# Performance work log

Measured on AMD Instinct MI355X. Metric: run time of the kernel, lower is better.

## Reference

```python
import jax, jax.numpy as jnp
import numpy as np

N, C, T, V = 16, 64, 512, 25
R, O, S = 8, 64, 3  # rel_channels, out_channels, num_subset


def setup_inputs() -> dict:
    key = jax.random.key(0)
    ks = jax.random.split(key, 12)
    sc = 0.05
    return {
        "x": jax.random.normal(ks[0], (N, C, T, V), jnp.float32),
        "A": jax.random.normal(ks[1], (S, V, V), jnp.float32) * 0.1,
        "alpha": jax.random.normal(ks[2], (1,), jnp.float32) * 0.1,
        "w1": jax.random.normal(ks[3], (S, R, C), jnp.float32) * sc,
        "b1": jax.random.normal(ks[4], (S, R), jnp.float32) * sc,
        "w2": jax.random.normal(ks[5], (S, R, C), jnp.float32) * sc,
        "b2": jax.random.normal(ks[6], (S, R), jnp.float32) * sc,
        "w3": jax.random.normal(ks[7], (S, O, C), jnp.float32) * sc,
        "b3": jax.random.normal(ks[8], (S, O), jnp.float32) * sc,
        "w4": jax.random.normal(ks[9], (S, O, R), jnp.float32) * sc,
        "b4": jax.random.normal(ks[10], (S, O), jnp.float32) * sc,
        "sparse": 0,
    }


def _mask(w, thr):
    # SparseConv2d: magnitude-threshold the 1x1 conv weights at runtime.
    return jnp.where(jnp.abs(w) > thr, w, jnp.zeros_like(w))


def reference(x, A, alpha, w1, b1, w2, b2, w3, b3, w4, b4, sparse):
    thr = jnp.float32(sparse)

    def conv1x1(w, b, inp):  # w [o,c], b [o], inp [n,c,t,v] -> [n,o,t,v]
        return jnp.einsum('oc,nctv->notv', _mask(w, thr), inp) + b[None, :, None, None]

    y = None
    for i in range(A.shape[0]):
        x1 = conv1x1(w1[i], b1[i], x).mean(-2)          # [n,r,v]
        x2 = conv1x1(w2[i], b2[i], x).mean(-2)          # [n,r,v]
        x3 = conv1x1(w3[i], b3[i], x)                   # [n,o,t,v]
        att = jnp.tanh(x1[..., :, None] - x2[..., None, :])  # [n,r,v,v]
        a = jnp.einsum('or,nruv->nouv', _mask(w4[i], thr), att) + b4[i][None, :, None, None]
        a = a * alpha + A[i][None, None]                # [n,o,v,v]
        z = jnp.einsum('ncuv,nctu->nctv', a, x3)        # node aggregation
        y = z if y is None else y + z
    # in_channels == out_channels -> residual is identity
    return jax.nn.relu(y + x)
```

## Files before the change

### kernel.cpp

```cpp
#include <hip/hip_runtime.h>
#include <cmath>

typedef __bf16 bf16x4v __attribute__((ext_vector_type(4)));
typedef __bf16 bf16x8 __attribute__((ext_vector_type(8)));
typedef float f32x4 __attribute__((ext_vector_type(4)));

namespace {
constexpr int kN = 16, kC = 64, kT = 512, kV = 25, kS = 3, kO = 64;
constexpr int kTV = kT * kV;
constexpr size_t WS_AFRAG = 102400;
constexpr size_t WS_W3F = WS_AFRAG + (size_t)48 * 131072;
constexpr size_t WS_XBF = WS_W3F + 3 * 8192;
}

__device__ __forceinline__ int swzB16(int c, int t, int ubyte) {
  return (c << 10) + (((t << 6) + ubyte) ^ ((((c ^ t) & 7)) << 4));
}

__global__ __launch_bounds__(256) void k1_cvt(const float* __restrict__ x,
                                              __bf16* __restrict__ xbf,
                                              float* __restrict__ xm) {
  const int bid = blockIdx.x;
  __shared__ float part[250][4];
  const int tid = threadIdx.x;
  const float4* xg4 = (const float4*)(x + (size_t)bid * kTV);
  bf16x4v* xb4 = (bf16x4v*)(xbf + (size_t)bid * kTV);
  if (tid < 250) {
    float a0 = 0.f, a1 = 0.f, a2 = 0.f, a3 = 0.f;
    for (int j = tid; j < 3200; j += 250) {
      float4 v = xg4[j];
      a0 += v.x; a1 += v.y; a2 += v.z; a3 += v.w;
      bf16x4v o;
      o[0] = (__bf16)v.x; o[1] = (__bf16)v.y;
      o[2] = (__bf16)v.z; o[3] = (__bf16)v.w;
      xb4[j] = o;
    }
    part[tid][0] = a0; part[tid][1] = a1; part[tid][2] = a2; part[tid][3] = a3;
  }
  __syncthreads();
  if (tid < 25) {
    float s = 0.f;
#pragma unroll
    for (int r = 0; r < 4; ++r) {
      int q = ((tid - r + 25) % 25) * 19 % 25;
#pragma unroll
      for (int p = 0; p < 10; ++p) s += part[q + 25 * p][r];
    }
    xm[bid * 25 + tid] = s * (1.f / 512.f);
  }
}

__global__ __launch_bounds__(256) void k2_attn(
    const float* __restrict__ xm, const float* __restrict__ Ag,
    const float* __restrict__ alpha, const float* __restrict__ w1,
    const float* __restrict__ b1, const float* __restrict__ w2,
    const float* __restrict__ b2, const float* __restrict__ w3,
    const float* __restrict__ w4, const float* __restrict__ b4,
    const int* __restrict__ sparse, unsigned char* __restrict__ ws) {
  const float thr = (float)sparse[0];
  const int b = blockIdx.x;
  const int s = b >> 6, n = (b >> 2) & 15, q = b & 3;
  __shared__ float xm_l[1600];
  __shared__ float x1_l[200], x2_l[200];
  __shared__ float att_l[8 * 625];
  __shared__ float attsum_l[200];
  __shared__ float ag_l[625];
  __shared__ float acs_l[25];
  __shared__ float w4_l[512];
  const int tid = threadIdx.x;
  for (int i = tid; i < 1600; i += 256) xm_l[i] = xm[n * 1600 + i];
  for (int i = tid; i < 512; i += 256) {
    float w = w4[s * 512 + i];
    w4_l[i] = (fabsf(w) > thr) ? w : 0.f;
  }
  for (int i = tid; i < 625; i += 256) ag_l[i] = Ag[s * 625 + i];
  __syncthreads();
  for (int i = tid; i < 400; i += 256) {
    int which = i / 200, idx = i % 200, r = idx / 25, u = idx % 25;
    const float* wrow = (which == 0 ? w1 : w2) + (s * 8 + r) * 64;
    float acc = 0.f;
    for (int cc = 0; cc < 64; ++cc) {
      float w = wrow[cc];
      w = (fabsf(w) > thr) ? w : 0.f;
      acc += w * xm_l[cc * 25 + u];
    }
    acc += (which == 0 ? b1 : b2)[s * 8 + r];
    if (which == 0) x1_l[idx] = acc;
    else x2_l[idx] = acc;
  }
  __syncthreads();
  for (int i = tid; i < 8 * 625; i += 256) {
    int r = i / 625, uv = i % 625, u = uv / 25, v = uv % 25;
    att_l[i] = tanhf(x1_l[r * 25 + u] - x2_l[r * 25 + v]);
  }
  __syncthreads();
  if (tid < 200) {
    int r = tid / 25, v = tid % 25;
    float sum = 0.f;
    for (int u = 0; u < 25; ++u) sum += att_l[r * 625 + u * 25 + v];
    attsum_l[tid] = sum;
  } else if (tid < 225) {
    int v = tid - 200;
    float sum = 0.f;
    for (int u = 0; u < 25; ++u) sum += ag_l[u * 25 + v];
    acs_l[v] = sum;
  }
  __syncthreads();
  const float al = alpha[0];
  unsigned char* afrag = ws + WS_AFRAG + (size_t)(s * 16 + n) * 131072;
  for (int slot = q * 2048 + tid; slot < (q + 1) * 2048; slot += 256) {
    int c = slot >> 7, vt = (slot >> 6) & 1, l = slot & 63;
    int v = vt * 16 + (l & 15), g = l >> 4;
    bf16x8 out;
    if (v < 25) {
      float b4v = b4[s * 64 + c];
#pragma unroll
      for (int j = 0; j < 8; ++j) {
        int u = g * 8 + j;
        float val = 0.f;
        if (u < 25) {
          float acc = 0.f;
#pragma unroll
          for (int r = 0; r < 8; ++r) acc += w4_l[c * 8 + r] * att_l[r * 625 + u * 25 + v];
          val = al * (acc + b4v) + ag_l[u * 25 + v];
        } else if (u == 25) {
          float acc = 0.f;
#pragma unroll
          for (int r = 0; r < 8; ++r) acc += w4_l[c * 8 + r] * attsum_l[r * 25 + v];
          val = al * acc + 25.f * al * b4v + acs_l[v];
        }
        out[j] = (__bf16)val;
      }
    } else {
#pragma unroll
      for (int j = 0; j < 8; ++j) out[j] = (__bf16)0.f;
    }
    *(bf16x8*)(afrag + (size_t)slot * 16) = out;
  }
  if (n == 0 && tid < 128) {
    unsigned char* w3f = ws + WS_W3F + (size_t)s * 8192;
    int slot = q * 128 + tid;
    int ot = slot >> 7, ks = (slot >> 6) & 1, l = slot & 63;
    int o = ot * 16 + (l & 15), g = l >> 4;
    bf16x8 out;
#pragma unroll
    for (int j = 0; j < 8; ++j) {
      int cp = ks * 32 + g * 8 + j;
      float w = w3[(s * 64 + o) * 64 + cp];
      out[j] = (__bf16)((fabsf(w) > thr) ? w : 0.f);
    }
    *(bf16x8*)(w3f + slot * 16) = out;
  }
}

__global__ __launch_bounds__(512) void k3_main(const __bf16* __restrict__ xbf,
                                               const float* __restrict__ b3,
                                               const unsigned char* __restrict__ ws,
                                               float* __restrict__ y) {
  const int n = blockIdx.x;
  const int tb = blockIdx.y;
  extern __shared__ __align__(16) unsigned char smem[];
  const int tid = threadIdx.x;
  const int w = tid >> 6, l = tid & 63, g = l >> 4, l15 = l & 15;

  {
    const f32x4* src = (const f32x4*)(ws + WS_W3F);
    f32x4* dst = (f32x4*)(smem + 65536);
    for (int i = tid; i < 1536; i += 512) dst[i] = src[i];
  }
  for (int idx = tid; idx < 3072; idx += 512) {
    int pair = idx / 3, k = idx % 3;
    int c = pair >> 4, t = pair & 15;
    *(unsigned int*)(smem + swzB16(c, t, 52 + 4 * k)) = 0u;
  }

  bf16x8 xa[4][2];
#pragma unroll
  for (int cti = 0; cti < 4; ++cti)
#pragma unroll
    for (int kf = 0; kf < 2; ++kf)
#pragma unroll
      for (int j = 0; j < 8; ++j) xa[cti][kf][j] = (__bf16)0.f;
  {
    const __bf16* xbp = xbf + (size_t)n * kC * kTV;
#pragma unroll
    for (int cti = 0; cti < 4; ++cti) {
      int tt = tb * 16 + 2 * w + (cti >> 1);
      int u = (cti & 1) * 16 + l15;
      if (u < 25) {
#pragma unroll
        for (int kf = 0; kf < 2; ++kf)
#pragma unroll
          for (int j = 0; j < 8; ++j) {
            int cp = kf * 32 + g * 8 + j;
            xa[cti][kf][j] = xbp[(size_t)cp * kTV + tt * 25 + u];
          }
      }
    }
  }
  __syncthreads();

  const unsigned char* afrag = ws + WS_AFRAG;

  f32x4 zacc[8][2];
#pragma unroll
  for (int cc = 0; cc < 8; ++cc)
#pragma unroll
    for (int vt = 0; vt < 2; ++vt) {
      f32x4 zz = {0.f, 0.f, 0.f, 0.f};
      zacc[cc][vt] = zz;
    }

  for (int s = 0; s < kS; ++s) {
    bf16x8 B2[8][2];
    const unsigned char* af = afrag + (size_t)(s * 16 + n) * 131072;
#pragma unroll
    for (int cc = 0; cc < 8; ++cc) {
      int c = w * 8 + cc;
#pragma unroll
      for (int vt = 0; vt < 2; ++vt)
        B2[cc][vt] = *(const bf16x8*)(af + ((c * 2 + vt) * 64 + l) * 16);
    }
    if (s) __syncthreads();

    const unsigned char* w3l = smem + 65536 + s * 8192;
#pragma unroll
    for (int ot = 0; ot < 4; ++ot) {
      bf16x8 wk0 = *(const bf16x8*)(w3l + ((ot * 2 + 0) * 64 + l) * 16);
      bf16x8 wk1 = *(const bf16x8*)(w3l + ((ot * 2 + 1) * 64 + l) * 16);
      int c = ot * 16 + l15;
#pragma unroll
      for (int cti = 0; cti < 4; ++cti) {
        f32x4 d = {0.f, 0.f, 0.f, 0.f};
        d = __builtin_amdgcn_mfma_f32_16x16x32_bf16(xa[cti][0], wk0, d, 0, 0, 0);
        d = __builtin_amdgcn_mfma_f32_16x16x32_bf16(xa[cti][1], wk1, d, 0, 0, 0);
        int tt = 2 * w + (cti >> 1);
        if (!(cti & 1)) {
          bf16x4v pk;
          pk[0] = (__bf16)d[0]; pk[1] = (__bf16)d[1];
          pk[2] = (__bf16)d[2]; pk[3] = (__bf16)d[3];
          *(bf16x4v*)(smem + swzB16(c, tt, g * 8)) = pk;
        } else if (g < 2) {
          bf16x4v pk;
          pk[0] = (__bf16)d[0]; pk[1] = (__bf16)d[1];
          pk[2] = (__bf16)d[2]; pk[3] = (__bf16)d[3];
          *(bf16x4v*)(smem + swzB16(c, tt, 32 + g * 8)) = pk;
        } else if (g == 2) {
          *(__bf16*)(smem + swzB16(c, tt, 48)) = (__bf16)d[0];
        }
      }
    }
    for (int i = tid; i < 1024; i += 512) {
      int c = i >> 4, t = i & 15;
      *(__bf16*)(smem + swzB16(c, t, 50)) = (__bf16)b3[s * 64 + c];
    }
    __syncthreads();
#pragma unroll
    for (int cc = 0; cc < 8; ++cc) {
      int c = w * 8 + cc;
      bf16x8 a2 = *(const bf16x8*)(smem + swzB16(c, l15, g * 16));
      zacc[cc][0] = __builtin_amdgcn_mfma_f32_16x16x32_bf16(a2, B2[cc][0], zacc[cc][0], 0, 0, 0);
      zacc[cc][1] = __builtin_amdgcn_mfma_f32_16x16x32_bf16(a2, B2[cc][1], zacc[cc][1], 0, 0, 0);
    }
  }
  __syncthreads();
  float* zs = (float*)smem;
  const __bf16* xbp = xbf + (size_t)n * kC * kTV;
  float4* yg4 = (float4*)(y + (size_t)n * kC * kTV);
#pragma unroll
  for (int h = 0; h < 2; ++h) {
    if ((w >> 2) == h) {
      int c0l = (w & 3) * 8;
#pragma unroll
      for (int cc = 0; cc < 8; ++cc)
#pragma unroll
        for (int vt = 0; vt < 2; ++vt) {
          int v = vt * 16 + l15;
          if (v < 25) {
#pragma unroll
            for (int jj = 0; jj < 4; ++jj)
              zs[(c0l + cc) * 400 + (g * 4 + jj) * 25 + v] = zacc[cc][vt][jj];
          }
        }
    }
    __syncthreads();
    for (int i4 = tid; i4 < 3200; i4 += 512) {
      int cl = i4 / 100, r4 = i4 % 100, c = h * 32 + cl;
      bf16x4v xv = *(const bf16x4v*)(xbp + (size_t)c * kTV + tb * 400 + r4 * 4);
      f32x4 zv = *(const f32x4*)(zs + cl * 400 + r4 * 4);
      float4 o;
      o.x = fmaxf(zv[0] + (float)xv[0], 0.f);
      o.y = fmaxf(zv[1] + (float)xv[1], 0.f);
      o.z = fmaxf(zv[2] + (float)xv[2], 0.f);
      o.w = fmaxf(zv[3] + (float)xv[3], 0.f);
      yg4[c * 3200 + tb * 100 + r4] = o;
    }
    __syncthreads();
  }
}

extern "C" void kernel_launch(void* const* d_in, const int* in_sizes, int n_in,
                              void* d_out, int out_size, void* d_ws, size_t ws_size,
                              hipStream_t stream) {
  const float* x = (const float*)d_in[0];
  const float* Ag = (const float*)d_in[1];
  const float* alpha = (const float*)d_in[2];
  const float* w1 = (const float*)d_in[3];
  const float* b1 = (const float*)d_in[4];
  const float* w2 = (const float*)d_in[5];
  const float* b2 = (const float*)d_in[6];
  const float* w3 = (const float*)d_in[7];
  const float* b3 = (const float*)d_in[8];
  const float* w4 = (const float*)d_in[9];
  const float* b4 = (const float*)d_in[10];
  const int* sparse = (const int*)d_in[11];

  unsigned char* ws = (unsigned char*)d_ws;
  float* xm = (float*)ws;
  __bf16* xbf = (__bf16*)(ws + WS_XBF);
  float* y = (float*)d_out;

  hipFuncSetAttribute((const void*)k3_main,
                      hipFuncAttributeMaxDynamicSharedMemorySize, 90112);

  k1_cvt<<<kN * kC, 256, 0, stream>>>(x, xbf, xm);
  k2_attn<<<kS * kN * 4, 256, 0, stream>>>(xm, Ag, alpha, w1, b1, w2, b2, w3, w4,
                                           b4, sparse, ws);
  dim3 g3(kN, kT / 16);
  k3_main<<<g3, 512, 90112, stream>>>(xbf, b3, ws, y);
}
```

Before: 74.68 us.

## Transpose x to channel-contiguous bf16 layout for vectorized MFMA operand loads

New measurement: 86.41 us. 15.7% more time.

```diff
diff --git a/kernel.cpp b/kernel.cpp
--- a/kernel.cpp
+++ b/kernel.cpp
@@ -10,53 +10,58 @@
 constexpr int kTV = kT * kV;
 constexpr size_t WS_AFRAG = 102400;
 constexpr size_t WS_W3F = WS_AFRAG + (size_t)48 * 131072;
-constexpr size_t WS_XBF = WS_W3F + 3 * 8192;
+constexpr size_t WS_XTR = WS_W3F + 3 * 8192;
+constexpr size_t WS_PSUM = WS_XTR + (size_t)16 * 819200 * 2 + 4096;
 }
 
 __device__ __forceinline__ int swzB16(int c, int t, int ubyte) {
   return (c << 10) + (((t << 6) + ubyte) ^ ((((c ^ t) & 7)) << 4));
 }
 
-__global__ __launch_bounds__(256) void k1_cvt(const float* __restrict__ x,
-                                              __bf16* __restrict__ xbf,
-                                              float* __restrict__ xm) {
-  const int bid = blockIdx.x;
-  __shared__ float part[250][4];
+__global__ __launch_bounds__(512) void k1_tr(const float* __restrict__ x,
+                                             unsigned char* __restrict__ ws) {
+  const int n = blockIdx.x, tc = blockIdx.y;
+  extern __shared__ __align__(16) unsigned char sm1[];
+  __bf16* tile = (__bf16*)sm1;
   const int tid = threadIdx.x;
-  const float4* xg4 = (const float4*)(x + (size_t)bid * kTV);
-  bf16x4v* xb4 = (bf16x4v*)(xbf + (size_t)bid * kTV);
-  if (tid < 250) {
-    float a0 = 0.f, a1 = 0.f, a2 = 0.f, a3 = 0.f;
-    for (int j = tid; j < 3200; j += 250) {
-      float4 v = xg4[j];
-      a0 += v.x; a1 += v.y; a2 += v.z; a3 += v.w;
-      bf16x4v o;
-      o[0] = (__bf16)v.x; o[1] = (__bf16)v.y;
-      o[2] = (__bf16)v.z; o[3] = (__bf16)v.w;
-      xb4[j] = o;
-    }
-    part[tid][0] = a0; part[tid][1] = a1; part[tid][2] = a2; part[tid][3] = a3;
-  }
-  __syncthreads();
-  if (tid < 25) {
+  const float4* xg4 = (const float4*)(x + (size_t)n * kC * kTV);
+  for (int i4 = tid; i4 < 12800; i4 += 512) {
+    int c = i4 / 200, r = i4 % 200;
+    float4 v = xg4[c * 3200 + tc * 200 + r];
+    bf16x4v o;
+    o[0] = (__bf16)v.x; o[1] = (__bf16)v.y;
+    o[2] = (__bf16)v.z; o[3] = (__bf16)v.w;
+    *(bf16x4v*)(tile + c * 800 + r * 4) = o;
+  }
+  __syncthreads();
+  __bf16* xtr = (__bf16*)(ws + WS_XTR) + (size_t)n * 819200 + (size_t)tc * 51200;
+  for (int col = tid; col < 800; col += 512) {
+    __bf16* dst = xtr + (size_t)col * 64;
+#pragma unroll
+    for (int cb = 0; cb < 8; ++cb) {
+      bf16x8 pk;
+#pragma unroll
+      for (int j = 0; j < 8; ++j) pk[j] = tile[(cb * 8 + j) * 800 + col];
+      *(bf16x8*)(dst + cb * 8) = pk;
+    }
+  }
+  float* psum = (float*)(ws + WS_PSUM);
+  for (int i = tid; i < 1600; i += 512) {
+    int c = i / 25, v = i % 25;
     float s = 0.f;
 #pragma unroll
-    for (int r = 0; r < 4; ++r) {
-      int q = ((tid - r + 25) % 25) * 19 % 25;
-#pragma unroll
-      for (int p = 0; p < 10; ++p) s += part[q + 25 * p][r];
-    }
-    xm[bid * 25 + tid] = s * (1.f / 512.f);
+    for (int t = 0; t < 32; ++t) s += (float)tile[c * 800 + t * 25 + v];
+    psum[((size_t)n * 1600 + i) * 16 + tc] = s;
   }
 }
 
 __global__ __launch_bounds__(256) void k2_attn(
-    const float* __restrict__ xm, const float* __restrict__ Ag,
-    const float* __restrict__ alpha, const float* __restrict__ w1,
-    const float* __restrict__ b1, const float* __restrict__ w2,
-    const float* __restrict__ b2, const float* __restrict__ w3,
-    const float* __restrict__ w4, const float* __restrict__ b4,
-    const int* __restrict__ sparse, unsigned char* __restrict__ ws) {
+    const float* __restrict__ Ag, const float* __restrict__ alpha,
+    const float* __restrict__ w1, const float* __restrict__ b1,
+    const float* __restrict__ w2, const float* __restrict__ b2,
+    const float* __restrict__ w3, const float* __restrict__ w4,
+    const float* __restrict__ b4, const int* __restrict__ sparse,
+    unsigned char* __restrict__ ws) {
   const float thr = (float)sparse[0];
   const int b = blockIdx.x;
   const int s = b >> 6, n = (b >> 2) & 15, q = b & 3;
@@ -68,7 +73,17 @@
   __shared__ float acs_l[25];
   __shared__ float w4_l[512];
   const int tid = threadIdx.x;
-  for (int i = tid; i < 1600; i += 256) xm_l[i] = xm[n * 1600 + i];
+  const float* psum = (const float*)(ws + WS_PSUM);
+  for (int i = tid; i < 1600; i += 256) {
+    const float4* p = (const float4*)(psum + ((size_t)n * 1600 + i) * 16);
+    float acc = 0.f;
+#pragma unroll
+    for (int qq = 0; qq < 4; ++qq) {
+      float4 v = p[qq];
+      acc += v.x + v.y + v.z + v.w;
+    }
+    xm_l[i] = acc * (1.f / 512.f);
+  }
   for (int i = tid; i < 512; i += 256) {
     float w = w4[s * 512 + i];
     w4_l[i] = (fabsf(w) > thr) ? w : 0.f;
@@ -153,7 +168,7 @@
   }
 }
 
-__global__ __launch_bounds__(512) void k3_main(const __bf16* __restrict__ xbf,
+__global__ __launch_bounds__(512) void k3_main(const float* __restrict__ x,
                                                const float* __restrict__ b3,
                                                const unsigned char* __restrict__ ws,
                                                float* __restrict__ y) {
@@ -174,28 +189,20 @@
     *(unsigned int*)(smem + swzB16(c, t, 52 + 4 * k)) = 0u;
   }
 
+  const unsigned char* xt = ws + WS_XTR + (size_t)n * 1638400 +
+                            (size_t)(tb >> 1) * 102400 + (size_t)(tb & 1) * 51200;
   bf16x8 xa[4][2];
 #pragma unroll
-  for (int cti = 0; cti < 4; ++cti)
-#pragma unroll
-    for (int kf = 0; kf < 2; ++kf)
-#pragma unroll
-      for (int j = 0; j < 8; ++j) xa[cti][kf][j] = (__bf16)0.f;
-  {
-    const __bf16* xbp = xbf + (size_t)n * kC * kTV;
-#pragma unroll
-    for (int cti = 0; cti < 4; ++cti) {
-      int tt = tb * 16 + 2 * w + (cti >> 1);
-      int u = (cti & 1) * 16 + l15;
-      if (u < 25) {
-#pragma unroll
-        for (int kf = 0; kf < 2; ++kf)
-#pragma unroll
-          for (int j = 0; j < 8; ++j) {
-            int cp = kf * 32 + g * 8 + j;
-            xa[cti][kf][j] = xbp[(size_t)cp * kTV + tt * 25 + u];
-          }
-      }
+  for (int cti = 0; cti < 4; ++cti) {
+    int t = 2 * w + (cti >> 1);
+    int u = (cti & 1) * 16 + l15;
+    if (u < 25) {
+      const unsigned char* bp = xt + (size_t)(t * 25 + u) * 128;
+      xa[cti][0] = *(const bf16x8*)(bp + g * 16);
+      xa[cti][1] = *(const bf16x8*)(bp + 64 + g * 16);
+    } else {
+#pragma unroll
+      for (int j = 0; j < 8; ++j) { xa[cti][0][j] = (__bf16)0.f; xa[cti][1][j] = (__bf16)0.f; }
     }
   }
   __syncthreads();
@@ -265,7 +272,7 @@
   }
   __syncthreads();
   float* zs = (float*)smem;
-  const __bf16* xbp = xbf + (size_t)n * kC * kTV;
+  const float4* xg4 = (const float4*)(x + (size_t)n * kC * kTV);
   float4* yg4 = (float4*)(y + (size_t)n * kC * kTV);
 #pragma unroll
   for (int h = 0; h < 2; ++h) {
@@ -286,13 +293,13 @@
     __syncthreads();
     for (int i4 = tid; i4 < 3200; i4 += 512) {
       int cl = i4 / 100, r4 = i4 % 100, c = h * 32 + cl;
-      bf16x4v xv = *(const bf16x4v*)(xbp + (size_t)c * kTV + tb * 400 + r4 * 4);
+      float4 xv = xg4[c * 3200 + tb * 100 + r4];
       f32x4 zv = *(const f32x4*)(zs + cl * 400 + r4 * 4);
       float4 o;
-      o.x = fmaxf(zv[0] + (float)xv[0], 0.f);
-      o.y = fmaxf(zv[1] + (float)xv[1], 0.f);
-      o.z = fmaxf(zv[2] + (float)xv[2], 0.f);
-      o.w = fmaxf(zv[3] + (float)xv[3], 0.f);
+      o.x = fmaxf(zv[0] + xv.x, 0.f);
+      o.y = fmaxf(zv[1] + xv.y, 0.f);
+      o.z = fmaxf(zv[2] + xv.z, 0.f);
+      o.w = fmaxf(zv[3] + xv.w, 0.f);
       yg4[c * 3200 + tb * 100 + r4] = o;
     }
     __syncthreads();
@@ -316,16 +323,17 @@
   const int* sparse = (const int*)d_in[11];
 
   unsigned char* ws = (unsigned char*)d_ws;
-  float* xm = (float*)ws;
-  __bf16* xbf = (__bf16*)(ws + WS_XBF);
   float* y = (float*)d_out;
 
+  hipFuncSetAttribute((const void*)k1_tr,
+                      hipFuncAttributeMaxDynamicSharedMemorySize, 102400);
   hipFuncSetAttribute((const void*)k3_main,
                       hipFuncAttributeMaxDynamicSharedMemorySize, 90112);
 
-  k1_cvt<<<kN * kC, 256, 0, stream>>>(x, xbf, xm);
-  k2_attn<<<kS * kN * 4, 256, 0, stream>>>(xm, Ag, alpha, w1, b1, w2, b2, w3, w4,
+  dim3 g1(kN, kT / 32);
+  k1_tr<<<g1, 512, 102400, stream>>>(x, ws);
+  k2_attn<<<kS * kN * 4, 256, 0, stream>>>(Ag, alpha, w1, b1, w2, b2, w3, w4,
                                            b4, sparse, ws);
   dim3 g3(kN, kT / 16);
-  k3_main<<<g3, 512, 90112, stream>>>(xbf, b3, ws, y);
-}
+  k3_main<<<g3, 512, 90112, stream>>>(x, b3, ws, y);
+}
```
